# Kernel tuning notes

Hardware: AMD Instinct MI355X
Metric: run time of the kernel (lower is better)

## Reference

```python
import jax, jax.numpy as jnp
import numpy as np

B, H, W = 1, 352, 1216
T = 6          # prop_time
CG = 8         # guidance channels per step
K = 9          # 3x3 propagation kernel


def _conv(x, w, b, pad, groups=1):
    out = jax.lax.conv_general_dilated(
        x, w, (1, 1), [(pad, pad), (pad, pad)],
        dimension_numbers=('NCHW', 'OIHW', 'NCHW'),
        feature_group_count=groups)
    return out if b is None else out + b[None, :, None, None]


def setup_inputs() -> dict:
    key = jax.random.key(0)
    ks = iter(jax.random.split(key, 32))
    def r(shape, s=0.1):
        return jax.random.normal(next(ks), shape, jnp.float32) * s
    return dict(
        feat_init=r((B, 1, H, W), 1.0),
        guidance=r((B, T * CG, H, W), 1.0),
        attn=r((B, 16, H, W), 1.0),
        feat_fix=r((B, 1, H, W), 1.0),
        aff_w_w=r((T, K, CG, 3, 3)), aff_w_b=r((T, K)),
        aff_o_w=r((T, 2 * (K - 1), CG, 3, 3)), aff_o_b=r((T, 2 * (K - 1))),
        proj_w=r((6, 3, 1, 1)),
        bn_gamma=jnp.ones((6,), jnp.float32), bn_beta=jnp.zeros((6,), jnp.float32),
        bn_mean=jnp.zeros((6,), jnp.float32), bn_var=jnp.ones((6,), jnp.float32),
        lsk0_w=r((22, 1, 1, 1)), lsk0_b=r((22,)),
        lsks_w=r((22, 1, 3, 3)), lsks_b=r((22,)),
        lsk1_w=r((11, 22, 1, 1)), lsk1_b=r((11,)),
        lsk2_w=r((11, 22, 1, 1)), lsk2_b=r((11,)),
        lsksq_w=r((2, 2, 3, 3)), lsksq_b=r((2,)),
        lskc_w=r((3, 11, 1, 1)), lskc_b=r((3,)),
    )


def _forward(feat_init, guidance, attn,
             aff_w_w, aff_w_b, aff_o_w, aff_o_b,
             proj_w, bn_gamma, bn_beta, bn_mean, bn_var,
             lsk0_w, lsk0_b, lsks_w, lsks_b, lsk1_w, lsk1_b,
             lsk2_w, lsk2_b, lsksq_w, lsksq_b, lskc_w, lskc_b):
    Bs, _, Hs, Ws = feat_init.shape
    # split guidance into T chunks of CG channels -> (T,B,CG,H,W)
    g = guidance.reshape(Bs, T, CG, Hs, Ws).transpose(1, 0, 2, 3, 4)

    def aff_fn(g_t, ww, wb, ow, ob):
        w = jax.nn.sigmoid(_conv(g_t, ww, wb, 1))              # (B,9,H,W)
        w = w / (w.sum(1, keepdims=True) + 1e-8)
        o = _conv(g_t, ow, ob, 1).reshape(Bs, K - 1, 2, Hs, Ws)
        zero = jnp.zeros((Bs, 1, 2, Hs, Ws), o.dtype)          # reference pixel
        o = jnp.concatenate([o[:, :4], zero, o[:, 4:]], 1).reshape(Bs, 2 * K, Hs, Ws)
        return o, w

    offs, affs = jax.vmap(aff_fn)(g, aff_w_w, aff_w_b, aff_o_w, aff_o_b)

    # modulated deformable conv, weight = ones(1,1,3,3), bias = 0, stride=1, pad=1
    ky = (jnp.repeat(jnp.arange(3), 3) - 1).astype(feat_init.dtype)  # (9,)
    kx = (jnp.tile(jnp.arange(3), 3) - 1).astype(feat_init.dtype)
    yy = jnp.arange(Hs, dtype=feat_init.dtype)
    xx = jnp.arange(Ws, dtype=feat_init.dtype)
    bidx = jnp.arange(Bs)[:, None, None, None]

    def dcn(feat, off, aff):
        img = feat[:, 0]                                       # (B,H,W)
        ys = yy[None, None, :, None] + ky[None, :, None, None] + off[:, 0::2]
        xs = xx[None, None, None, :] + kx[None, :, None, None] + off[:, 1::2]
        y0 = jnp.floor(ys); x0 = jnp.floor(xs)
        wy = ys - y0; wx = xs - x0
        y0i = y0.astype(jnp.int32); x0i = x0.astype(jnp.int32)
        def g4(yi, xi):
            valid = (yi >= 0) & (yi < Hs) & (xi >= 0) & (xi < Ws)
            v = img[bidx, jnp.clip(yi, 0, Hs - 1), jnp.clip(xi, 0, Ws - 1)]
            return v * valid.astype(v.dtype)
        samp = (g4(y0i, x0i) * (1 - wy) * (1 - wx)
                + g4(y0i, x0i + 1) * (1 - wy) * wx
                + g4(y0i + 1, x0i) * wy * (1 - wx)
                + g4(y0i + 1, x0i + 1) * wy * wx)
        return (aff * samp).sum(1)[:, None]                    # (B,1,H,W)

    def step(f, ox):
        o, a = ox
        fn = dcn(f, o, a)
        return fn, fn

    _, feats = jax.lax.scan(step, feat_init.astype(jnp.float32), (offs, affs))

    # combine(list_feat[3:6], attn)
    x3 = jnp.concatenate([feats[3], feats[4], feats[5]], 1)    # (B,3,H,W)
    sf = _conv(x3, proj_w, None, 0)                            # conv 3->6, no bias
    sf = (sf - bn_mean[None, :, None, None]) * jax.lax.rsqrt(bn_var + 1e-5)[None, :, None, None] \
         * bn_gamma[None, :, None, None] + bn_beta[None, :, None, None]
    sf = jnp.where(sf >= 0, sf, 0.2 * sf)                      # LeakyReLU(0.2)
    x22 = jnp.concatenate([attn, sf], 1)                       # (B,22,H,W)

    a1 = _conv(x22, lsk0_w, lsk0_b, 0, 22)                     # depthwise 1x1
    a2 = _conv(a1, lsks_w, lsks_b, 1, 22)                      # depthwise 3x3
    a1 = _conv(a1, lsk1_w, lsk1_b, 0)                          # 22->11
    a2 = _conv(a2, lsk2_w, lsk2_b, 0)                          # 22->11
    cat = jnp.concatenate([a1, a2], 1)
    agg = jnp.concatenate([cat.mean(1, keepdims=True), cat.max(1, keepdims=True)], 1)
    sig = jax.nn.sigmoid(_conv(agg, lsksq_w, lsksq_b, 1))
    at = a1 * sig[:, 0:1] + a2 * sig[:, 1:2]
    at = _conv(at, lskc_w, lskc_b, 0)                          # 11->3
    return (x3 * at).sum(1, keepdims=True)                     # (B,1,H,W)


def reference(feat_init, guidance, attn, feat_fix,
              aff_w_w, aff_w_b, aff_o_w, aff_o_b,
              proj_w, bn_gamma, bn_beta, bn_mean, bn_var,
              lsk0_w, lsk0_b, lsks_w, lsks_b, lsk1_w, lsk1_b,
              lsk2_w, lsk2_b, lsksq_w, lsksq_b, lskc_w, lskc_b):
    # feat_fix only feeds an unused mask path (if False branch) in the original
    return _forward(feat_init, guidance, attn,
                    aff_w_w, aff_w_b, aff_o_w, aff_o_b,
                    proj_w, bn_gamma, bn_beta, bn_mean, bn_var,
                    lsk0_w, lsk0_b, lsks_w, lsks_b, lsk1_w, lsk1_b,
                    lsk2_w, lsk2_b, lsksq_w, lsksq_b, lskc_w, lskc_b)
```

## Files before the change

### kernel.cpp

```cpp
#include <hip/hip_runtime.h>
#include <hip/hip_bf16.h>

#define HH 352
#define WW 1216
#define HWSZ (HH * WW)
#define TT 6

#define WS_CW   16
#define WS_TW   11008
#define WS_FB   12032

typedef __attribute__((ext_vector_type(4))) float f32x4;
typedef __attribute__((ext_vector_type(8))) short s16x8;
union FU { unsigned int u[4]; s16x8 v; };

__device__ inline float ld_in(const void* p, long long i, int bf) {
    return bf ? __bfloat162float(((const __hip_bfloat16*)p)[i]) : ((const float*)p)[i];
}

__device__ inline unsigned int bfsplit_pack(float v) {
    unsigned int uv = __float_as_uint(v);
    unsigned int h = (uv + 0x7FFFu + ((uv >> 16) & 1u)) >> 16;
    float hf = __uint_as_float(h << 16);
    float r = v - hf;
    unsigned int ur = __float_as_uint(r);
    unsigned int l = (ur + 0x7FFFu + ((ur >> 16) & 1u)) >> 16;
    return (h & 0xFFFFu) | (l << 16);
}

__device__ inline int detect_mode(const void* guid) {
    const unsigned int* u = (const unsigned int*)guid;
    int cnt = 0;
    for (int i = 0; i < 128; ++i) {
        unsigned int lo = u[i] & 0xFFFFu;
        int e = (int)((lo >> 7) & 0xFF);
        if (e >= 110 && e <= 140) cnt++;
    }
    return (cnt >= 96) ? 1 : 0;
}

__global__ __launch_bounds__(256) void prep_all(
        const void* feat_init, const void* guid,
        const void* aww, const void* awb, const void* aow, const void* aob,
        const void* projw, const void* bng, const void* bnb,
        const void* bnm, const void* bnv,
        const void* l0w, const void* l0b, const void* lsw, const void* lsb,
        const void* l1w, const void* l1b, const void* l2w, const void* l2b,
        const void* sqw, const void* sqb, const void* lcw, const void* lcb,
        float* ws) {
    __shared__ int smode;
    if (threadIdx.x == 0) {
        int mode = detect_mode(guid);
        smode = mode;
        if (blockIdx.x == 0) *(int*)ws = mode;
    }
    __syncthreads();
    const int bf = smode;
    {
        int i = blockIdx.x * 256 + threadIdx.x;
        if (i < HWSZ) ws[WS_FB + 6 * HWSZ + i] = ld_in(feat_init, i, bf);
    }
    if (blockIdx.x >= 32) return;
    const int tid = blockIdx.x * 256 + threadIdx.x;
    const int stp = 32 * 256;
    float* cw = ws + WS_CW;
    for (int idx = tid; idx < TT * 9 * 72; idx += stp) {
        int t = idx / 648; int r = idx % 648;
        int co = r / 72; int ci = (r % 72) / 9; int tap = r % 9;
        cw[t * 1825 + 25 + co * 72 + ci * 9 + tap] = ld_in(aww, idx, bf);
    }
    for (int idx = tid; idx < TT * 16 * 72; idx += stp) {
        int t = idx / 1152; int r = idx % 1152;
        int co = r / 72; int ci = (r % 72) / 9; int tap = r % 9;
        cw[t * 1825 + 25 + (9 + co) * 72 + ci * 9 + tap] = ld_in(aow, idx, bf);
    }
    for (int idx = tid; idx < TT * 9; idx += stp)
        cw[(idx / 9) * 1825 + (idx % 9)] = ld_in(awb, idx, bf);
    for (int idx = tid; idx < TT * 16; idx += stp)
        cw[(idx / 16) * 1825 + 9 + (idx % 16)] = ld_in(aob, idx, bf);

    float* tw = ws + WS_TW;
    for (int i = tid; i < 18; i += stp) tw[i] = ld_in(projw, i, bf);
    for (int i = tid; i < 6; i += stp) {
        float sc = ld_in(bng, i, bf) * rsqrtf(ld_in(bnv, i, bf) + 1e-5f);
        tw[18 + i] = sc;
        tw[24 + i] = ld_in(bnb, i, bf) - ld_in(bnm, i, bf) * sc;
    }
    for (int i = tid; i < 22;  i += stp) tw[32  + i] = ld_in(l0w, i, bf);
    for (int i = tid; i < 22;  i += stp) tw[54  + i] = ld_in(l0b, i, bf);
    for (int i = tid; i < 198; i += stp) tw[76  + i] = ld_in(lsw, i, bf);
    for (int i = tid; i < 22;  i += stp) tw[274 + i] = ld_in(lsb, i, bf);
    for (int i = tid; i < 242; i += stp) tw[296 + i] = ld_in(l1w, i, bf);
    for (int i = tid; i < 11;  i += stp) tw[538 + i] = ld_in(l1b, i, bf);
    for (int i = tid; i < 242; i += stp) tw[549 + i] = ld_in(l2w, i, bf);
    for (int i = tid; i < 11;  i += stp) tw[791 + i] = ld_in(l2b, i, bf);
    for (int i = tid; i < 36;  i += stp) tw[802 + i] = ld_in(sqw, i, bf);
    for (int i = tid; i < 2;   i += stp) tw[838 + i] = ld_in(sqb, i, bf);
    for (int i = tid; i < 33;  i += stp) tw[840 + i] = ld_in(lcw, i, bf);
    for (int i = tid; i < 3;   i += stp) tw[873 + i] = ld_in(lcb, i, bf);
}

__device__ inline float samp(const float* __restrict__ src, int y, int x) {
    bool valid = (y >= 0) & (y < HH) & (x >= 0) & (x < WW);
    int yc = min(max(y, 0), HH - 1);
    int xc = min(max(x, 0), WW - 1);
    float v = src[yc * WW + xc];
    return valid ? v : 0.0f;
}

__global__ __launch_bounds__(256) void dcn_fused(
        const void* __restrict__ guid, const int* __restrict__ flagp,
        const float* __restrict__ wts,
        const float* __restrict__ src, float* __restrict__ dst, int t) {
    __shared__ unsigned int hal[8][10][36];
    __shared__ float outb[4][2][16][27];
    const int bf = *flagp;
    const int bx = blockIdx.x % 38, by = blockIdx.x / 38;
    const int x0 = bx * 32, y0 = by * 8;

    if (!bf) {
        const float* gp = (const float*)guid + (long long)(t * 8) * HWSZ;
        for (int idx = threadIdx.x; idx < 800; idx += 256) {
            int ci = idx / 100; int rem = idx % 100; int rr = rem / 10; int k = rem % 10;
            int gy = y0 - 1 + rr;
            int gxb = x0 - 4 + 4 * k;
            float vx = 0.f, vy = 0.f, vz = 0.f, vw = 0.f;
            if (gy >= 0 && gy < HH) {
                const float* rowp = gp + (long long)ci * HWSZ + (long long)gy * WW;
                if (gxb >= 0 && gxb + 3 < WW) {
                    const float4 v4 = *(const float4*)(rowp + gxb);
                    vx = v4.x; vy = v4.y; vz = v4.z; vw = v4.w;
                } else {
                    if (gxb + 0 >= 0 && gxb + 0 < WW) vx = rowp[gxb + 0];
                    if (gxb + 1 >= 0 && gxb + 1 < WW) vy = rowp[gxb + 1];
                    if (gxb + 2 >= 0 && gxb + 2 < WW) vz = rowp[gxb + 2];
                    if (gxb + 3 >= 0 && gxb + 3 < WW) vw = rowp[gxb + 3];
                }
            }
            int c0 = 4 * k - 3;
            if (c0 + 0 >= 0 && c0 + 0 < 36) hal[ci][rr][c0 + 0] = bfsplit_pack(vx);
            if (c0 + 1 >= 0 && c0 + 1 < 36) hal[ci][rr][c0 + 1] = bfsplit_pack(vy);
            if (c0 + 2 >= 0 && c0 + 2 < 36) hal[ci][rr][c0 + 2] = bfsplit_pack(vz);
            if (c0 + 3 >= 0 && c0 + 3 < 36) hal[ci][rr][c0 + 3] = bfsplit_pack(vw);
        }
    } else {
        for (int idx = threadIdx.x; idx < 8 * 360; idx += 256) {
            int ci = idx / 360; int r = (idx % 360) / 36; int c = idx % 36;
            int gy = y0 - 1 + r, gx = x0 - 1 + c;
            float v = 0.f;
            if (c < 34 && gy >= 0 && gy < HH && gx >= 0 && gx < WW)
                v = ld_in(guid, (long long)(t * 8 + ci) * HWSZ + gy * WW + gx, bf);
            hal[ci][r][c] = bfsplit_pack(v);
        }
    }
    const int lane = threadIdx.x & 63;
    const int wave = threadIdx.x >> 6;
    const int col = lane & 15, g = lane >> 4;

    FU Bh[2][3], Bl[2][3];
#pragma unroll
    for (int Nt = 0; Nt < 2; ++Nt)
#pragma unroll
    for (int c = 0; c < 3; ++c) {
        unsigned short eh[8], el[8];
#pragma unroll
        for (int j = 0; j < 8; ++j) {
            int ci = 2 * g + (j >> 2), dx = j & 3;
            int cc = Nt * 16 + col;
            float w = 0.f;
            if (cc < 25 && dx < 3) w = wts[25 + cc * 72 + ci * 9 + c * 3 + dx];
            unsigned int pk = bfsplit_pack(w);
            eh[j] = (unsigned short)(pk & 0xFFFFu);
            el[j] = (unsigned short)(pk >> 16);
        }
#pragma unroll
        for (int q = 0; q < 4; ++q) {
            Bh[Nt][c].u[q] = (unsigned int)eh[2*q] | ((unsigned int)eh[2*q+1] << 16);
            Bl[Nt][c].u[q] = (unsigned int)el[2*q] | ((unsigned int)el[2*q+1] << 16);
        }
    }
    __syncthreads();

    const float* bias = wts;
#pragma unroll
    for (int m = 0; m < 4; ++m) {
        const int M = wave * 4 + m;
        const int py = M >> 1;
        const int xoff = (M & 1) * 16;
        const int pxx = xoff + col;
        FU Ah[3], Al[3];
#pragma unroll
        for (int c = 0; c < 3; ++c) {
            const unsigned int* r0 = &hal[2 * g][py + c][pxx];
            const unsigned int* r1 = &hal[2 * g + 1][py + c][pxx];
            unsigned int q0 = r0[0], q1 = r0[1], q2 = r0[2], q3 = r0[3];
            unsigned int q4 = r1[0], q5 = r1[1], q6 = r1[2], q7 = r1[3];
            Ah[c].u[0] = __builtin_amdgcn_perm(q1, q0, 0x05040100u);
            Ah[c].u[1] = __builtin_amdgcn_perm(q3, q2, 0x05040100u);
            Ah[c].u[2] = __builtin_amdgcn_perm(q5, q4, 0x05040100u);
            Ah[c].u[3] = __builtin_amdgcn_perm(q7, q6, 0x05040100u);
            Al[c].u[0] = __builtin_amdgcn_perm(q1, q0, 0x07060302u);
            Al[c].u[1] = __builtin_amdgcn_perm(q3, q2, 0x07060302u);
            Al[c].u[2] = __builtin_amdgcn_perm(q5, q4, 0x07060302u);
            Al[c].u[3] = __builtin_amdgcn_perm(q7, q6, 0x07060302u);
        }
#pragma unroll
        for (int Nt = 0; Nt < 2; ++Nt) {
            f32x4 acc = {0.f, 0.f, 0.f, 0.f};
#pragma unroll
            for (int c = 0; c < 3; ++c) {
                acc = __builtin_amdgcn_mfma_f32_16x16x32_bf16(Ah[c].v, Bh[Nt][c].v, acc, 0, 0, 0);
                acc = __builtin_amdgcn_mfma_f32_16x16x32_bf16(Al[c].v, Bh[Nt][c].v, acc, 0, 0, 0);
                acc = __builtin_amdgcn_mfma_f32_16x16x32_bf16(Ah[c].v, Bl[Nt][c].v, acc, 0, 0, 0);
            }
            const int co = Nt * 16 + col;
            if (co < 25) {
                float bs = bias[co];
#pragma unroll
                for (int r = 0; r < 4; ++r)
                    outb[wave][m & 1][g * 4 + r][co] = acc[r] + bs;
            }
        }
        {
            const int px = col;
            const int gy = y0 + py;
            const int gx = x0 + xoff + px;
            const float* ob = &outb[wave][m & 1][px][0];
            float sg[3], oyv[3], oxv[3];
            float psum = 0.f;
#pragma unroll
            for (int i = 0; i < 3; ++i) {
                int tap = i * 4 + g;
                bool valid = tap < 9;
                int tc = valid ? tap : 8;
                float wv = ob[tc];
                float sgv = 1.f / (1.f + __expf(-wv));
                sg[i] = valid ? sgv : 0.f;
                psum += sg[i];
                int kp = (tap < 4) ? tap : tap - 1;
                kp = min(kp, 7);
                float oy = ob[9 + 2 * kp];
                float ox = ob[10 + 2 * kp];
                bool use_off = valid && (tap != 4);
                oyv[i] = use_off ? oy : 0.f;
                oxv[i] = use_off ? ox : 0.f;
            }
            psum += __shfl_xor(psum, 16);
            psum += __shfl_xor(psum, 32);
            const float inv = 1.f / (psum + 1e-8f);
            float out = 0.f;
#pragma unroll
            for (int i = 0; i < 3; ++i) {
                int tap = min(i * 4 + g, 8);
                float w = sg[i] * inv;
                int d3 = tap / 3;
                int dy = d3 - 1, dx = tap - 3 * d3 - 1;
                float ys = (float)(gy + dy) + oyv[i];
                float xs = (float)(gx + dx) + oxv[i];
                float yf = floorf(ys), xf = floorf(xs);
                float wy = ys - yf, wx = xs - xf;
                int yi = (int)yf, xi = (int)xf;
                float v00 = samp(src, yi, xi);
                float v01 = samp(src, yi, xi + 1);
                float v10 = samp(src, yi + 1, xi);
                float v11 = samp(src, yi + 1, xi + 1);
                float sv = v00 * (1.f - wy) * (1.f - wx) + v01 * (1.f - wy) * wx
                         + v10 * wy * (1.f - wx) + v11 * wy * wx;
                out = fmaf(w, sv, out);
            }
            out += __shfl_xor(out, 16);
            out += __shfl_xor(out, 32);
            if (g == 0) dst[gy * WW + gx] = out;
        }
    }
}

__global__ __launch_bounds__(256) void tail1(
        const void* __restrict__ attn, const int* __restrict__ flagp,
        const float* __restrict__ tw, const float* __restrict__ feats,
        float* __restrict__ a1) {
    const int bf = *flagp;
    const int p = blockIdx.x * 256 + threadIdx.x;
    float x3[3] = { feats[3 * HWSZ + p], feats[4 * HWSZ + p], feats[5 * HWSZ + p] };
    float sf[6];
#pragma unroll
    for (int j = 0; j < 6; ++j) {
        float v = tw[j * 3 + 0] * x3[0] + tw[j * 3 + 1] * x3[1] + tw[j * 3 + 2] * x3[2];
        v = v * tw[18 + j] + tw[24 + j];
        sf[j] = (v >= 0.0f) ? v : 0.2f * v;
    }
#pragma unroll
    for (int c = 0; c < 22; ++c) {
        float x = (c < 16) ? ld_in(attn, (long long)c * HWSZ + p, bf) : sf[c - 16];
        a1[c * HWSZ + p] = fmaf(x, tw[32 + c], tw[54 + c]);
    }
}

__global__ __launch_bounds__(256) void tail2(
        const float* __restrict__ tw, const float* __restrict__ a1,
        float* __restrict__ a11, float* __restrict__ a21, float* __restrict__ agg) {
    __shared__ float tile[10][34];
    const int bx = blockIdx.x % 38, by = blockIdx.x / 38;
    const int x0 = bx * 32, y0 = by * 8;
    const int lx = threadIdx.x % 32, ly = threadIdx.x / 32;
    float acc1[11], acc2[11];
#pragma unroll
    for (int j = 0; j < 11; ++j) { acc1[j] = tw[538 + j]; acc2[j] = tw[791 + j]; }
    for (int c = 0; c < 22; ++c) {
        __syncthreads();
        for (int idx = threadIdx.x; idx < 340; idx += 256) {
            int r = idx / 34, cc = idx % 34;
            int gy = y0 - 1 + r, gx = x0 - 1 + cc;
            tile[r][cc] = (gy >= 0 && gy < HH && gx >= 0 && gx < WW)
                          ? a1[c * HWSZ + gy * WW + gx] : 0.0f;
        }
        __syncthreads();
        float a1c = tile[ly + 1][lx + 1];
        float a2c = tw[274 + c];
#pragma unroll
        for (int dy = 0; dy < 3; ++dy)
#pragma unroll
            for (int dx = 0; dx < 3; ++dx)
                a2c = fmaf(tile[ly + dy][lx + dx], tw[76 + c * 9 + dy * 3 + dx], a2c);
#pragma unroll
        for (int j = 0; j < 11; ++j) {
            acc1[j] = fmaf(a1c, tw[296 + j * 22 + c], acc1[j]);
            acc2[j] = fmaf(a2c, tw[549 + j * 22 + c], acc2[j]);
        }
    }
    const int p = (y0 + ly) * WW + x0 + lx;
    float s = 0.0f, mx = -1e30f;
#pragma unroll
    for (int j = 0; j < 11; ++j) {
        a11[j * HWSZ + p] = acc1[j];
        a21[j * HWSZ + p] = acc2[j];
        s += acc1[j] + acc2[j];
        mx = fmaxf(mx, fmaxf(acc1[j], acc2[j]));
    }
    agg[p] = s * (1.0f / 22.0f);
    agg[HWSZ + p] = mx;
}

__global__ __launch_bounds__(256) void tail3(
        const int* __restrict__ flagp, const float* __restrict__ tw,
        const float* __restrict__ feats,
        const float* __restrict__ a11, const float* __restrict__ a21,
        const float* __restrict__ agg, void* __restrict__ out) {
    __shared__ float t0[10][34], t1[10][34];
    const int bx = blockIdx.x % 38, by = blockIdx.x / 38;
    const int x0 = bx * 32, y0 = by * 8;
    for (int idx = threadIdx.x; idx < 340; idx += 256) {
        int r = idx / 34, cc = idx % 34;
        int gy = y0 - 1 + r, gx = x0 - 1 + cc;
        bool ok = (gy >= 0 && gy < HH && gx >= 0 && gx < WW);
        t0[r][cc] = ok ? agg[gy * WW + gx] : 0.0f;
        t1[r][cc] = ok ? agg[HWSZ + gy * WW + gx] : 0.0f;
    }
    __syncthreads();
    const int lx = threadIdx.x % 32, ly = threadIdx.x / 32;
    float s0 = tw[838], s1 = tw[839];
#pragma unroll
    for (int dy = 0; dy < 3; ++dy)
#pragma unroll
        for (int dx = 0; dx < 3; ++dx) {
            float v0 = t0[ly + dy][lx + dx], v1 = t1[ly + dy][lx + dx];
            s0 = fmaf(v0, tw[802 + 0 * 18 + 0 * 9 + dy * 3 + dx], s0);
            s0 = fmaf(v1, tw[802 + 0 * 18 + 1 * 9 + dy * 3 + dx], s0);
            s1 = fmaf(v0, tw[802 + 1 * 18 + 0 * 9 + dy * 3 + dx], s1);
            s1 = fmaf(v1, tw[802 + 1 * 18 + 1 * 9 + dy * 3 + dx], s1);
        }
    float sg0 = 1.0f / (1.0f + __expf(-s0));
    float sg1 = 1.0f / (1.0f + __expf(-s1));
    const int p = (y0 + ly) * WW + x0 + lx;
    float at3[3] = { tw[873], tw[874], tw[875] };
#pragma unroll
    for (int j = 0; j < 11; ++j) {
        float at = a11[j * HWSZ + p] * sg0 + a21[j * HWSZ + p] * sg1;
#pragma unroll
        for (int i = 0; i < 3; ++i) at3[i] = fmaf(at, tw[840 + i * 11 + j], at3[i]);
    }
    float o = feats[3 * HWSZ + p] * at3[0] + feats[4 * HWSZ + p] * at3[1]
            + feats[5 * HWSZ + p] * at3[2];
    int bf = *flagp;
    if (bf) ((__hip_bfloat16*)out)[p] = __float2bfloat16(o);
    else    ((float*)out)[p] = o;
}

extern "C" void kernel_launch(void* const* d_in, const int* in_sizes, int n_in,
                              void* d_out, int out_size, void* d_ws, size_t ws_size,
                              hipStream_t stream) {
    (void)in_sizes; (void)n_in; (void)out_size; (void)ws_size;
    float* WSF = (float*)d_ws;
    const int* flagp = (const int*)d_ws;
    float* cw   = WSF + WS_CW;
    float* tw   = WSF + WS_TW;
    float* FB   = WSF + WS_FB;
    float* A1   = FB + 7 * HWSZ;
    float* A11  = A1 + 22 * HWSZ;
    float* A21  = A11 + 11 * HWSZ;
    float* AGG  = A21 + 11 * HWSZ;

    prep_all<<<1672, 256, 0, stream>>>(d_in[0], d_in[1],
        d_in[4], d_in[5], d_in[6], d_in[7],
        d_in[8], d_in[9], d_in[10], d_in[11], d_in[12],
        d_in[13], d_in[14], d_in[15], d_in[16],
        d_in[17], d_in[18], d_in[19], d_in[20],
        d_in[21], d_in[22], d_in[23], d_in[24], WSF);

    for (int t = 0; t < 6; ++t) {
        const float* src = (t == 0) ? (FB + 6 * HWSZ) : (FB + (t - 1) * HWSZ);
        dcn_fused<<<44 * 38, 256, 0, stream>>>(d_in[1], flagp, cw + t * 1825, src, FB + t * HWSZ, t);
    }
    tail1<<<HWSZ / 256, 256, 0, stream>>>(d_in[2], flagp, tw, FB, A1);
    tail2<<<44 * 38, 256, 0, stream>>>(tw, A1, A11, A21, AGG);
    tail3<<<44 * 38, 256, 0, stream>>>(flagp, tw, FB, A11, A21, AGG, d_out);
}
```

Before: 464.6 us.

## Precompute MFMA weight fragments, specialize interior halo loads, fuse tail1 into tail2

Weight B-fragments (bf16 hi/lo split) are now built once in the prep kernel and stored in workspace, so each dcn block loads them as uint4 instead of recomputing the split per block. Interior tiles skip the bounds checks when loading the guidance halo. tail1 is merged into tail2: the 22-channel a1 tensor is computed on the fly into shared memory, which removes a full-resolution global round trip and one launch. The cost is a larger shared-memory footprint in the fused tail kernel, which may lower occupancy.

```diff
diff --git a/kernel.cpp b/kernel.cpp
--- a/kernel.cpp
+++ b/kernel.cpp
@@ -8,7 +8,8 @@
 
 #define WS_CW   16
 #define WS_TW   11008
-#define WS_FB   12032
+#define WS_BF   12032
+#define WS_FB   30464
 
 typedef __attribute__((ext_vector_type(4))) float f32x4;
 typedef __attribute__((ext_vector_type(8))) short s16x8;
@@ -63,21 +64,46 @@
     if (blockIdx.x >= 32) return;
     const int tid = blockIdx.x * 256 + threadIdx.x;
     const int stp = 32 * 256;
+
     float* cw = ws + WS_CW;
-    for (int idx = tid; idx < TT * 9 * 72; idx += stp) {
-        int t = idx / 648; int r = idx % 648;
-        int co = r / 72; int ci = (r % 72) / 9; int tap = r % 9;
-        cw[t * 1825 + 25 + co * 72 + ci * 9 + tap] = ld_in(aww, idx, bf);
-    }
-    for (int idx = tid; idx < TT * 16 * 72; idx += stp) {
-        int t = idx / 1152; int r = idx % 1152;
-        int co = r / 72; int ci = (r % 72) / 9; int tap = r % 9;
-        cw[t * 1825 + 25 + (9 + co) * 72 + ci * 9 + tap] = ld_in(aow, idx, bf);
-    }
     for (int idx = tid; idx < TT * 9; idx += stp)
-        cw[(idx / 9) * 1825 + (idx % 9)] = ld_in(awb, idx, bf);
+        cw[(idx / 9) * 32 + (idx % 9)] = ld_in(awb, idx, bf);
     for (int idx = tid; idx < TT * 16; idx += stp)
-        cw[(idx / 16) * 1825 + 9 + (idx % 16)] = ld_in(aob, idx, bf);
+        cw[(idx / 16) * 32 + 9 + (idx % 16)] = ld_in(aob, idx, bf);
+
+    uint4* bfb = (uint4*)(ws + WS_BF);
+    for (int idx = tid; idx < TT * 2 * 3 * 64; idx += stp) {
+        int t = idx / 384; int r = idx % 384;
+        int Nt = r / 192; int r2 = r % 192;
+        int c = r2 / 64; int lane = r2 % 64;
+        int col = lane & 15, g = lane >> 4;
+        unsigned short eh[8], el[8];
+#pragma unroll
+        for (int j = 0; j < 8; ++j) {
+            int ci = 2 * g + (j >> 2), dx = j & 3;
+            int cc = Nt * 16 + col;
+            float w = 0.f;
+            if (cc < 25 && dx < 3) {
+                if (cc < 9) w = ld_in(aww, (long long)(((t * 9 + cc) * 8 + ci) * 9 + c * 3 + dx), bf);
+                else        w = ld_in(aow, (long long)(((t * 16 + (cc - 9)) * 8 + ci) * 9 + c * 3 + dx), bf);
+            }
+            unsigned int pk = bfsplit_pack(w);
+            eh[j] = (unsigned short)(pk & 0xFFFFu);
+            el[j] = (unsigned short)(pk >> 16);
+        }
+        uint4 H, L;
+        H.x = (unsigned int)eh[0] | ((unsigned int)eh[1] << 16);
+        H.y = (unsigned int)eh[2] | ((unsigned int)eh[3] << 16);
+        H.z = (unsigned int)eh[4] | ((unsigned int)eh[5] << 16);
+        H.w = (unsigned int)eh[6] | ((unsigned int)eh[7] << 16);
+        L.x = (unsigned int)el[0] | ((unsigned int)el[1] << 16);
+        L.y = (unsigned int)el[2] | ((unsigned int)el[3] << 16);
+        L.z = (unsigned int)el[4] | ((unsigned int)el[5] << 16);
+        L.w = (unsigned int)el[6] | ((unsigned int)el[7] << 16);
+        int base = t * 768 + (Nt * 3 + c) * 128;
+        bfb[base + lane] = H;
+        bfb[base + 64 + lane] = L;
+    }
 
     float* tw = ws + WS_TW;
     for (int i = tid; i < 18; i += stp) tw[i] = ld_in(projw, i, bf);
@@ -110,38 +136,60 @@
 
 __global__ __launch_bounds__(256) void dcn_fused(
         const void* __restrict__ guid, const int* __restrict__ flagp,
-        const float* __restrict__ wts,
+        const float* __restrict__ bias, const uint4* __restrict__ bfrag,
         const float* __restrict__ src, float* __restrict__ dst, int t) {
     __shared__ unsigned int hal[8][10][36];
     __shared__ float outb[4][2][16][27];
     const int bf = *flagp;
     const int bx = blockIdx.x % 38, by = blockIdx.x / 38;
     const int x0 = bx * 32, y0 = by * 8;
+    const bool interior = (by >= 1) && (by <= 42) && (bx >= 1) && (bx <= 36);
 
     if (!bf) {
         const float* gp = (const float*)guid + (long long)(t * 8) * HWSZ;
-        for (int idx = threadIdx.x; idx < 800; idx += 256) {
-            int ci = idx / 100; int rem = idx % 100; int rr = rem / 10; int k = rem % 10;
-            int gy = y0 - 1 + rr;
-            int gxb = x0 - 4 + 4 * k;
-            float vx = 0.f, vy = 0.f, vz = 0.f, vw = 0.f;
-            if (gy >= 0 && gy < HH) {
-                const float* rowp = gp + (long long)ci * HWSZ + (long long)gy * WW;
-                if (gxb >= 0 && gxb + 3 < WW) {
-                    const float4 v4 = *(const float4*)(rowp + gxb);
-                    vx = v4.x; vy = v4.y; vz = v4.z; vw = v4.w;
+        if (interior) {
+            for (int idx = threadIdx.x; idx < 800; idx += 256) {
+                int ci = idx / 100; int rem = idx % 100; int rr = rem / 10; int k = rem % 10;
+                const float* rowp = gp + (long long)ci * HWSZ + (long long)(y0 - 1 + rr) * WW;
+                const float4 v4 = *(const float4*)(rowp + (x0 - 4 + 4 * k));
+                int c0 = 4 * k - 3;
+                if (k == 0) {
+                    hal[ci][rr][0] = bfsplit_pack(v4.w);
+                } else if (k == 9) {
+                    hal[ci][rr][33] = bfsplit_pack(v4.x);
+                    hal[ci][rr][34] = bfsplit_pack(v4.y);
+                    hal[ci][rr][35] = bfsplit_pack(v4.z);
                 } else {
-                    if (gxb + 0 >= 0 && gxb + 0 < WW) vx = rowp[gxb + 0];
-                    if (gxb + 1 >= 0 && gxb + 1 < WW) vy = rowp[gxb + 1];
-                    if (gxb + 2 >= 0 && gxb + 2 < WW) vz = rowp[gxb + 2];
-                    if (gxb + 3 >= 0 && gxb + 3 < WW) vw = rowp[gxb + 3];
+                    hal[ci][rr][c0 + 0] = bfsplit_pack(v4.x);
+                    hal[ci][rr][c0 + 1] = bfsplit_pack(v4.y);
+                    hal[ci][rr][c0 + 2] = bfsplit_pack(v4.z);
+                    hal[ci][rr][c0 + 3] = bfsplit_pack(v4.w);
                 }
             }
-            int c0 = 4 * k - 3;
-            if (c0 + 0 >= 0 && c0 + 0 < 36) hal[ci][rr][c0 + 0] = bfsplit_pack(vx);
-            if (c0 + 1 >= 0 && c0 + 1 < 36) hal[ci][rr][c0 + 1] = bfsplit_pack(vy);
-            if (c0 + 2 >= 0 && c0 + 2 < 36) hal[ci][rr][c0 + 2] = bfsplit_pack(vz);
-            if (c0 + 3 >= 0 && c0 + 3 < 36) hal[ci][rr][c0 + 3] = bfsplit_pack(vw);
+        } else {
+            for (int idx = threadIdx.x; idx < 800; idx += 256) {
+                int ci = idx / 100; int rem = idx % 100; int rr = rem / 10; int k = rem % 10;
+                int gy = y0 - 1 + rr;
+                int gxb = x0 - 4 + 4 * k;
+                float vx = 0.f, vy = 0.f, vz = 0.f, vw = 0.f;
+                if (gy >= 0 && gy < HH) {
+                    const float* rowp = gp + (long long)ci * HWSZ + (long long)gy * WW;
+                    if (gxb >= 0 && gxb + 3 < WW) {
+                        const float4 v4 = *(const float4*)(rowp + gxb);
+                        vx = v4.x; vy = v4.y; vz = v4.z; vw = v4.w;
+                    } else {
+                        if (gxb + 0 >= 0 && gxb + 0 < WW) vx = rowp[gxb + 0];
+                        if (gxb + 1 >= 0 && gxb + 1 < WW) vy = rowp[gxb + 1];
+                        if (gxb + 2 >= 0 && gxb + 2 < WW) vz = rowp[gxb + 2];
+                        if (gxb + 3 >= 0 && gxb + 3 < WW) vw = rowp[gxb + 3];
+                    }
+                }
+                int c0 = 4 * k - 3;
+                if (c0 + 0 >= 0 && c0 + 0 < 36) hal[ci][rr][c0 + 0] = bfsplit_pack(vx);
+                if (c0 + 1 >= 0 && c0 + 1 < 36) hal[ci][rr][c0 + 1] = bfsplit_pack(vy);
+                if (c0 + 2 >= 0 && c0 + 2 < 36) hal[ci][rr][c0 + 2] = bfsplit_pack(vz);
+                if (c0 + 3 >= 0 && c0 + 3 < 36) hal[ci][rr][c0 + 3] = bfsplit_pack(vw);
+            }
         }
     } else {
         for (int idx = threadIdx.x; idx < 8 * 360; idx += 256) {
@@ -162,26 +210,14 @@
     for (int Nt = 0; Nt < 2; ++Nt)
 #pragma unroll
     for (int c = 0; c < 3; ++c) {
-        unsigned short eh[8], el[8];
-#pragma unroll
-        for (int j = 0; j < 8; ++j) {
-            int ci = 2 * g + (j >> 2), dx = j & 3;
-            int cc = Nt * 16 + col;
-            float w = 0.f;
-            if (cc < 25 && dx < 3) w = wts[25 + cc * 72 + ci * 9 + c * 3 + dx];
-            unsigned int pk = bfsplit_pack(w);
-            eh[j] = (unsigned short)(pk & 0xFFFFu);
-            el[j] = (unsigned short)(pk >> 16);
-        }
-#pragma unroll
-        for (int q = 0; q < 4; ++q) {
-            Bh[Nt][c].u[q] = (unsigned int)eh[2*q] | ((unsigned int)eh[2*q+1] << 16);
-            Bl[Nt][c].u[q] = (unsigned int)el[2*q] | ((unsigned int)el[2*q+1] << 16);
-        }
+        const uint4* bp = bfrag + (Nt * 3 + c) * 128;
+        uint4 H = bp[lane];
+        uint4 L = bp[64 + lane];
+        Bh[Nt][c].u[0] = H.x; Bh[Nt][c].u[1] = H.y; Bh[Nt][c].u[2] = H.z; Bh[Nt][c].u[3] = H.w;
+        Bl[Nt][c].u[0] = L.x; Bl[Nt][c].u[1] = L.y; Bl[Nt][c].u[2] = L.z; Bl[Nt][c].u[3] = L.w;
     }
     __syncthreads();
 
-    const float* bias = wts;
 #pragma unroll
     for (int m = 0; m < 4; ++m) {
         const int M = wave * 4 + m;
@@ -275,53 +311,85 @@
     }
 }
 
-__global__ __launch_bounds__(256) void tail1(
+__global__ __launch_bounds__(256) void tail2m(
         const void* __restrict__ attn, const int* __restrict__ flagp,
         const float* __restrict__ tw, const float* __restrict__ feats,
-        float* __restrict__ a1) {
+        float* __restrict__ a11, float* __restrict__ a21, float* __restrict__ agg) {
+    __shared__ float a1t[22][10][36];
+    __shared__ float ft[3][10][36];
     const int bf = *flagp;
-    const int p = blockIdx.x * 256 + threadIdx.x;
-    float x3[3] = { feats[3 * HWSZ + p], feats[4 * HWSZ + p], feats[5 * HWSZ + p] };
-    float sf[6];
-#pragma unroll
-    for (int j = 0; j < 6; ++j) {
-        float v = tw[j * 3 + 0] * x3[0] + tw[j * 3 + 1] * x3[1] + tw[j * 3 + 2] * x3[2];
-        v = v * tw[18 + j] + tw[24 + j];
-        sf[j] = (v >= 0.0f) ? v : 0.2f * v;
-    }
-#pragma unroll
-    for (int c = 0; c < 22; ++c) {
-        float x = (c < 16) ? ld_in(attn, (long long)c * HWSZ + p, bf) : sf[c - 16];
-        a1[c * HWSZ + p] = fmaf(x, tw[32 + c], tw[54 + c]);
-    }
-}
-
-__global__ __launch_bounds__(256) void tail2(
-        const float* __restrict__ tw, const float* __restrict__ a1,
-        float* __restrict__ a11, float* __restrict__ a21, float* __restrict__ agg) {
-    __shared__ float tile[10][34];
     const int bx = blockIdx.x % 38, by = blockIdx.x / 38;
     const int x0 = bx * 32, y0 = by * 8;
-    const int lx = threadIdx.x % 32, ly = threadIdx.x / 32;
+    const bool interior = (by >= 1) && (by <= 42) && (bx >= 1) && (bx <= 36);
+
+    if (!bf && interior) {
+        for (int idx = threadIdx.x; idx < 1900; idx += 256) {
+            int plane = idx / 100; int rem = idx % 100; int rr = rem / 10; int k = rem % 10;
+            const float* rowp;
+            float sc, bc;
+            if (plane < 16) {
+                rowp = (const float*)attn + (long long)plane * HWSZ + (long long)(y0 - 1 + rr) * WW;
+                sc = tw[32 + plane]; bc = tw[54 + plane];
+            } else {
+                rowp = feats + (long long)(3 + plane - 16) * HWSZ + (long long)(y0 - 1 + rr) * WW;
+                sc = 1.f; bc = 0.f;
+            }
+            const float4 v4 = *(const float4*)(rowp + (x0 - 4 + 4 * k));
+            float t0 = fmaf(v4.x, sc, bc), t1 = fmaf(v4.y, sc, bc);
+            float t2 = fmaf(v4.z, sc, bc), t3 = fmaf(v4.w, sc, bc);
+            float* drow = (plane < 16) ? &a1t[plane][rr][0] : &ft[plane - 16][rr][0];
+            int c0 = 4 * k - 3;
+            if (k == 0) {
+                drow[0] = t3;
+            } else if (k == 9) {
+                drow[33] = t0; drow[34] = t1; drow[35] = t2;
+            } else {
+                drow[c0 + 0] = t0; drow[c0 + 1] = t1; drow[c0 + 2] = t2; drow[c0 + 3] = t3;
+            }
+        }
+    } else {
+        for (int idx = threadIdx.x; idx < 19 * 360; idx += 256) {
+            int plane = idx / 360; int rem = idx % 360; int rr = rem / 36; int c = rem % 36;
+            int gy = y0 - 1 + rr, gx = x0 - 1 + c;
+            bool ok = (c < 34) && gy >= 0 && gy < HH && gx >= 0 && gx < WW;
+            if (plane < 16) {
+                float v = 0.f;
+                if (ok) v = fmaf(ld_in(attn, (long long)plane * HWSZ + gy * WW + gx, bf),
+                                 tw[32 + plane], tw[54 + plane]);
+                a1t[plane][rr][c] = v;
+            } else {
+                ft[plane - 16][rr][c] = ok ? feats[(long long)(3 + plane - 16) * HWSZ + gy * WW + gx] : 0.f;
+            }
+        }
+    }
+    __syncthreads();
+    for (int idx = threadIdx.x; idx < 6 * 340; idx += 256) {
+        int j = idx / 340; int r = (idx % 340) / 34; int cc = idx % 34;
+        int gy = y0 - 1 + r, gx = x0 - 1 + cc;
+        bool ok = (gy >= 0 && gy < HH && gx >= 0 && gx < WW);
+        float o = 0.f;
+        if (ok) {
+            float f0 = ft[0][r][cc], f1 = ft[1][r][cc], f2 = ft[2][r][cc];
+            float v = tw[j * 3 + 0] * f0 + tw[j * 3 + 1] * f1 + tw[j * 3 + 2] * f2;
+            v = v * tw[18 + j] + tw[24 + j];
+            v = (v >= 0.f) ? v : 0.2f * v;
+            o = fmaf(v, tw[32 + 16 + j], tw[54 + 16 + j]);
+        }
+        a1t[16 + j][r][cc] = o;
+    }
+    __syncthreads();
+    const int lx = threadIdx.x & 31, ly = threadIdx.x >> 5;
     float acc1[11], acc2[11];
 #pragma unroll
     for (int j = 0; j < 11; ++j) { acc1[j] = tw[538 + j]; acc2[j] = tw[791 + j]; }
     for (int c = 0; c < 22; ++c) {
-        __syncthreads();
-        for (int idx = threadIdx.x; idx < 340; idx += 256) {
-            int r = idx / 34, cc = idx % 34;
-            int gy = y0 - 1 + r, gx = x0 - 1 + cc;
-            tile[r][cc] = (gy >= 0 && gy < HH && gx >= 0 && gx < WW)
-                          ? a1[c * HWSZ + gy * WW + gx] : 0.0f;
-        }
-        __syncthreads();
-        float a1c = tile[ly + 1][lx + 1];
+        float a1c = a1t[c][ly + 1][lx + 1];
         float a2c = tw[274 + c];
 #pragma unroll
         for (int dy = 0; dy < 3; ++dy)
 #pragma unroll
-            for (int dx = 0; dx < 3; ++dx)
-                a2c = fmaf(tile[ly + dy][lx + dx], tw[76 + c * 9 + dy * 3 + dx], a2c);
+        for (int dx = 0; dx < 3; ++dx)
+            a2c = fmaf(a1t[c][ly + dy][lx + dx], tw[76 + c * 9 + dy * 3 + dx], a2c);
 #pragma unroll
         for (int j = 0; j < 11; ++j) {
             acc1[j] = fmaf(a1c, tw[296 + j * 22 + c], acc1[j]);
@@ -394,9 +462,9 @@
     const int* flagp = (const int*)d_ws;
     float* cw   = WSF + WS_CW;
     float* tw   = WSF + WS_TW;
+    const uint4* bfb = (const uint4*)(WSF + WS_BF);
     float* FB   = WSF + WS_FB;
-    float* A1   = FB + 7 * HWSZ;
-    float* A11  = A1 + 22 * HWSZ;
+    float* A11  = FB + 7 * HWSZ;
     float* A21  = A11 + 11 * HWSZ;
     float* AGG  = A21 + 11 * HWSZ;
 
@@ -409,9 +477,9 @@
 
     for (int t = 0; t < 6; ++t) {
         const float* src = (t == 0) ? (FB + 6 * HWSZ) : (FB + (t - 1) * HWSZ);
-        dcn_fused<<<44 * 38, 256, 0, stream>>>(d_in[1], flagp, cw + t * 1825, src, FB + t * HWSZ, t);
-    }
-    tail1<<<HWSZ / 256, 256, 0, stream>>>(d_in[2], flagp, tw, FB, A1);
-    tail2<<<44 * 38, 256, 0, stream>>>(tw, A1, A11, A21, AGG);
+        dcn_fused<<<44 * 38, 256, 0, stream>>>(d_in[1], flagp, cw + t * 32,
+                                               bfb + t * 768, src, FB + t * HWSZ, t);
+    }
+    tail2m<<<44 * 38, 256, 0, stream>>>(d_in[2], flagp, tw, FB, A11, A21, AGG);
     tail3<<<44 * 38, 256, 0, stream>>>(flagp, tw, FB, A11, A21, AGG, d_out);
 }
```

Result: faster. 404.3 us (-13.0%).
